# Optimization experiments

Measured on AMD Instinct MI355X. Metric: run time of the kernel, lower is better.

Reference implementation:

```python
import jax, jax.numpy as jnp
import numpy as np


def setup_inputs() -> dict:
    key = jax.random.key(0)
    ks = jax.random.split(key, 5)
    B, n_sites, d_bond, d_phys = 8192, 2048, 8, 2
    sr = n_sites // 2  # single_rank
    x = jax.random.normal(ks[0], (B, n_sites, d_phys), dtype=jnp.float32)
    scale = 0.01
    left_b = scale * jax.random.normal(ks[1], (d_bond, d_phys), dtype=jnp.float32)
    left = scale * jax.random.normal(ks[2], (sr - 1, d_bond, d_bond, d_phys), dtype=jnp.float32)
    right = scale * jax.random.normal(ks[3], (sr - 1, d_bond, d_bond, d_phys), dtype=jnp.float32)
    right_b = scale * jax.random.normal(ks[4], (d_bond, d_phys), dtype=jnp.float32)
    return {"x": x, "left_b": left_b, "left": left, "right": right, "right_b": right_b}


def reference(x, left_b, left, right, right_b):
    # x: [B, n_sites, d_phys]; left/right: [sr-1, bond, bond, d_phys]; boundaries: [bond, d_phys]
    n_sites = x.shape[1]
    sr = n_sites // 2

    # In-place slice normalizations performed at the top of call()
    left_b = left_b.at[2].set(left_b[2] / jnp.linalg.norm(left_b[2]))
    left = left.at[3].set(left[3] / jnp.linalg.norm(left[3]))
    right = right.at[3].set(right[3] / jnp.linalg.norm(right[3]))
    right_b = right_b.at[2].set(right_b[2] / jnp.linalg.norm(right_b[2]))

    # Left half: boundary phys contraction -> [B, bond]
    lvec = jnp.einsum("ap,kp->ka", left_b, x[:, 0])
    # Middle left: contract site-stack and phys axes -> [B, bond, bond]
    Lmat = jnp.einsum("sabp,ksp->kab", left, x[:, 1:sr])
    l = jnp.einsum("ka,kab->kb", lvec, Lmat)  # contract lb_n[0]^ln[1]

    # Right half (mirror)
    rvec = jnp.einsum("ap,kp->ka", right_b, x[:, n_sites - 1])
    Rmat = jnp.einsum("sabp,ksp->kab", right, x[:, sr : n_sites - 1])
    r = jnp.einsum("ka,kab->kb", rvec, Rmat)

    # Join halves: ln[2]^rn[2] -> scalar per sample, shape [B]
    return jnp.einsum("kb,kb->k", l, r)
```

## Files before the change

kernel.cpp:

```cpp
#include <hip/hip_runtime.h>
#include <hip/hip_bf16.h>

typedef __bf16  bf16x8  __attribute__((ext_vector_type(8)));
typedef float   floatx4 __attribute__((ext_vector_type(4)));

#define ROWLEN      4096
#define B_SAMPLES   8192
#define FRAG_ELEMS  (2*64*4*64*8)


__global__ __launch_bounds__(256) void repack_kernel(
    const float* __restrict__ left, const float* __restrict__ right,
    __bf16* __restrict__ wfrag)
{
    __shared__ float norms[2];
    const int tid  = threadIdx.x;
    const int wv   = tid >> 6;
    const int ln   = tid & 63;

    if (wv < 2) {
        const float* W = (wv == 0) ? left : right;
        float a = W[384 + ln], b = W[384 + 64 + ln];
        float s = a * a + b * b;
        s += __shfl_xor(s, 1);  s += __shfl_xor(s, 2);  s += __shfl_xor(s, 4);
        s += __shfl_xor(s, 8);  s += __shfl_xor(s, 16); s += __shfl_xor(s, 32);
        if (ln == 0) norms[wv] = 1.0f / sqrtf(s);
    }
    __syncthreads();
    const float invL = norms[0];
    const float invR = norms[1];

    const int g    = (int)(blockIdx.x * 256) + tid;
    const int lane = g & 63;
    const int nt   = (g >> 6) & 3;
    const int t    = (g >> 8) & 63;
    const int h    = (g >> 14) & 1;
    const int kk0  = t * 32 + (lane >> 4) * 8;
    const int n    = nt * 16 + (lane & 15);
    const int a    = n >> 3, bb = n & 7;
    const float* W = (h == 0) ? left : right;

    bf16x8 frag;
#pragma unroll
    for (int si = 0; si < 4; ++si) {
        const int kk = kk0 + si * 2;
        int s;  bool valid;
        if (h == 0) { s = (kk >> 1) - 1; valid = (kk >= 2); }
        else        { s = (kk >> 1);     valid = (s < 1023); }
        float w0 = 0.f, w1 = 0.f;
        if (valid) {
            const float* wp = W + ((s * 8 + a) * 8 + bb) * 2;
            w0 = wp[0]; w1 = wp[1];
            if (s == 3) { const float sc = (h == 0) ? invL : invR; w0 *= sc; w1 *= sc; }
        }
        frag[si * 2]     = (__bf16)w0;
        frag[si * 2 + 1] = (__bf16)w1;
    }
    ((bf16x8*)wfrag)[g] = frag;
}

__global__ __launch_bounds__(512, 4) void mps_main_kernel(
    const float* __restrict__ x, const __bf16* __restrict__ wfrag,
    const float* __restrict__ left_b, const float* __restrict__ right_b,
    float* __restrict__ out)
{
    __shared__ float lds[2][4][16][65];
    const int tid  = threadIdx.x;
    const int wid  = tid >> 6;
    const int lane = tid & 63;
    const int h    = wid & 1;
    const int c    = wid >> 1;
    const int mcol = lane & 15;
    const int q    = lane >> 4;
    const int blk  = blockIdx.x;

    const float* arow = x + (size_t)(blk * 16 + mcol) * ROWLEN
                          + h * 2048 + c * 512 + q * 8;
    const bf16x8* bbase = (const bf16x8*)wfrag
                          + ((size_t)(h * 64 + c * 16) * 4) * 64 + lane;

    floatx4 acc0 = {0.f,0.f,0.f,0.f}, acc1 = {0.f,0.f,0.f,0.f};
    floatx4 acc2 = {0.f,0.f,0.f,0.f}, acc3 = {0.f,0.f,0.f,0.f};

#pragma unroll 2
    for (int tl = 0; tl < 16; ++tl) {
        const floatx4* ap = (const floatx4*)(arow + tl * 32);
        const floatx4 a0 = __builtin_nontemporal_load(ap);
        const floatx4 a1 = __builtin_nontemporal_load(ap + 1);
        bf16x8 af;
        af[0] = (__bf16)a0[0]; af[1] = (__bf16)a0[1];
        af[2] = (__bf16)a0[2]; af[3] = (__bf16)a0[3];
        af[4] = (__bf16)a1[0]; af[5] = (__bf16)a1[1];
        af[6] = (__bf16)a1[2]; af[7] = (__bf16)a1[3];
        const bf16x8* bp = bbase + (size_t)tl * 256;
        const bf16x8 w0 = bp[0], w1 = bp[64], w2 = bp[128], w3 = bp[192];
        acc0 = __builtin_amdgcn_mfma_f32_16x16x32_bf16(af, w0, acc0, 0, 0, 0);
        acc1 = __builtin_amdgcn_mfma_f32_16x16x32_bf16(af, w1, acc1, 0, 0, 0);
        acc2 = __builtin_amdgcn_mfma_f32_16x16x32_bf16(af, w2, acc2, 0, 0, 0);
        acc3 = __builtin_amdgcn_mfma_f32_16x16x32_bf16(af, w3, acc3, 0, 0, 0);
    }

#pragma unroll
    for (int i = 0; i < 4; ++i) {
        const int r0 = q * 4 + i;
        lds[h][c][r0][ 0 + mcol] = acc0[i];
        lds[h][c][r0][16 + mcol] = acc1[i];
        lds[h][c][r0][32 + mcol] = acc2[i];
        lds[h][c][r0][48 + mcol] = acc3[i];
    }
    __syncthreads();

    if (tid < 128) {
        const int mm = tid >> 3;
        const int b  = tid & 7;
        const size_t k = (size_t)blk * 16 + mm;
        const float* xr = x + k * ROWLEN;
        const float x0 = xr[0],    x1 = xr[1];
        const float y0 = xr[4094], y1 = xr[4095];
        const float lbn = 1.0f / sqrtf(left_b[4]*left_b[4] + left_b[5]*left_b[5]);
        const float rbn = 1.0f / sqrtf(right_b[4]*right_b[4] + right_b[5]*right_b[5]);
        float l = 0.f, r = 0.f;
#pragma unroll
        for (int a = 0; a < 8; ++a) {
            float lv = left_b[a*2]  * x0 + left_b[a*2+1]  * x1;
            float rv = right_b[a*2] * y0 + right_b[a*2+1] * y1;
            if (a == 2) { lv *= lbn; rv *= rbn; }
            const int n = a * 8 + b;
            const float ls = lds[0][0][mm][n] + lds[0][1][mm][n]
                           + lds[0][2][mm][n] + lds[0][3][mm][n];
            const float rs = lds[1][0][mm][n] + lds[1][1][mm][n]
                           + lds[1][2][mm][n] + lds[1][3][mm][n];
            l += lv * ls;
            r += rv * rs;
        }
        float vv = l * r;
        vv += __shfl_xor(vv, 1);
        vv += __shfl_xor(vv, 2);
        vv += __shfl_xor(vv, 4);
        if (b == 0) out[k] = vv;
    }
}

extern "C" void kernel_launch(void* const* d_in, const int* in_sizes, int n_in,
                              void* d_out, int out_size, void* d_ws, size_t ws_size,
                              hipStream_t stream)
{
    const float* x       = (const float*)d_in[0];
    const float* left_b  = (const float*)d_in[1];
    const float* left    = (const float*)d_in[2];
    const float* right   = (const float*)d_in[3];
    const float* right_b = (const float*)d_in[4];

    __bf16* wfrag = (__bf16*)d_ws;
    float*  out   = (float*)d_out;

    hipLaunchKernelGGL(repack_kernel, dim3(128), dim3(256), 0, stream,
                       left, right, wfrag);
    hipLaunchKernelGGL(mps_main_kernel, dim3(B_SAMPLES / 16), dim3(512), 0, stream,
                       x, wfrag, left_b, right_b, out);
}
```

Measured before the change: 208.5 us.

## Stage x tiles into LDS with async global_load_lds double buffering

The main kernel now copies the x tile for each quarter-row into a double-buffered LDS buffer using direct global-to-LDS loads with XOR swizzling. The copy of the next chunk overlaps with MFMA compute on the current one. Work across waves changes from a split over halves and K to a split over N-tile and K-half, so the partial sums to reduce drop from four to two. LDS use grows to 128KB per block and launch bounds fall to 2 blocks per SM, which lowers occupancy and adds barrier synchronisation.

```diff
diff --git a/kernel.cpp b/kernel.cpp
--- a/kernel.cpp
+++ b/kernel.cpp
@@ -6,7 +6,13 @@
 
 #define ROWLEN      4096
 #define B_SAMPLES   8192
-#define FRAG_ELEMS  (2*64*4*64*8)
+
+typedef const __attribute__((address_space(1))) void* gas1_t;
+typedef __attribute__((address_space(3))) void*       las3_t;
+
+__device__ __forceinline__ void stage16(const float* g, float* l) {
+    __builtin_amdgcn_global_load_lds((gas1_t)g, (las3_t)l, 16, 0, 0);
+}
 
 
 __global__ __launch_bounds__(256) void repack_kernel(
@@ -59,61 +65,97 @@
     ((bf16x8*)wfrag)[g] = frag;
 }
 
-__global__ __launch_bounds__(512, 4) void mps_main_kernel(
+__global__ __launch_bounds__(512, 2) void mps_main_kernel(
     const float* __restrict__ x, const __bf16* __restrict__ wfrag,
     const float* __restrict__ left_b, const float* __restrict__ right_b,
     float* __restrict__ out)
 {
-    __shared__ float lds[2][4][16][65];
+    __shared__ float buf[2][16][1024];
     const int tid  = threadIdx.x;
     const int wid  = tid >> 6;
     const int lane = tid & 63;
-    const int h    = wid & 1;
-    const int c    = wid >> 1;
+    const int ntp  = wid & 3;
+    const int kkp  = wid >> 2;
     const int mcol = lane & 15;
     const int q    = lane >> 4;
+    const int sx   = mcol & 7;
     const int blk  = blockIdx.x;
 
-    const float* arow = x + (size_t)(blk * 16 + mcol) * ROWLEN
-                          + h * 2048 + c * 512 + q * 8;
-    const bf16x8* bbase = (const bf16x8*)wfrag
-                          + ((size_t)(h * 64 + c * 16) * 4) * 64 + lane;
-
-    floatx4 acc0 = {0.f,0.f,0.f,0.f}, acc1 = {0.f,0.f,0.f,0.f};
-    floatx4 acc2 = {0.f,0.f,0.f,0.f}, acc3 = {0.f,0.f,0.f,0.f};
-
-#pragma unroll 2
-    for (int tl = 0; tl < 16; ++tl) {
-        const floatx4* ap = (const floatx4*)(arow + tl * 32);
-        const floatx4 a0 = __builtin_nontemporal_load(ap);
-        const floatx4 a1 = __builtin_nontemporal_load(ap + 1);
-        bf16x8 af;
-        af[0] = (__bf16)a0[0]; af[1] = (__bf16)a0[1];
-        af[2] = (__bf16)a0[2]; af[3] = (__bf16)a0[3];
-        af[4] = (__bf16)a1[0]; af[5] = (__bf16)a1[1];
-        af[6] = (__bf16)a1[2]; af[7] = (__bf16)a1[3];
-        const bf16x8* bp = bbase + (size_t)tl * 256;
-        const bf16x8 w0 = bp[0], w1 = bp[64], w2 = bp[128], w3 = bp[192];
-        acc0 = __builtin_amdgcn_mfma_f32_16x16x32_bf16(af, w0, acc0, 0, 0, 0);
-        acc1 = __builtin_amdgcn_mfma_f32_16x16x32_bf16(af, w1, acc1, 0, 0, 0);
-        acc2 = __builtin_amdgcn_mfma_f32_16x16x32_bf16(af, w2, acc2, 0, 0, 0);
-        acc3 = __builtin_amdgcn_mfma_f32_16x16x32_bf16(af, w3, acc3, 0, 0, 0);
-    }
-
+    const float* xblk = x + (size_t)blk * 16 * ROWLEN;
+    const bf16x8* wf  = (const bf16x8*)wfrag;
+
+    auto STAGE = [&](int w, int b) {
+#pragma unroll
+        for (int rr = 0; rr < 2; ++rr) {
+            const int r = 2 * wid + rr;
+            const int sxor = r & 7;
+            const float* grow = xblk + (size_t)r * ROWLEN + w * 1024;
+#pragma unroll
+            for (int gi = 0; gi < 4; ++gi) {
+                const float* gp = grow + (gi * 64 + (lane ^ sxor)) * 4;
+                stage16(gp, &buf[b][r][gi * 256]);
+            }
+        }
+    };
+
+    floatx4 accL = {0.f,0.f,0.f,0.f};
+    floatx4 accR = {0.f,0.f,0.f,0.f};
+
+    auto COMPUTE = [&](int w, int b, floatx4& acc) {
+        const int h = w >> 1;
+#pragma unroll
+        for (int g4 = 0; g4 < 4; ++g4) {
+            bf16x8 wv[4];
+#pragma unroll
+            for (int j = 0; j < 4; ++j) {
+                const int t = (w & 1) * 32 + kkp * 16 + g4 * 4 + j;
+                wv[j] = wf[((size_t)((h * 64 + t) * 4 + ntp)) * 64 + lane];
+            }
+#pragma unroll
+            for (int j = 0; j < 4; ++j) {
+                const int tl = g4 * 4 + j;
+                const int gg = kkp * 128 + tl * 8 + 2 * q;
+                const floatx4 a0 = *(const floatx4*)&buf[b][mcol][((gg    ) ^ sx) * 4];
+                const floatx4 a1 = *(const floatx4*)&buf[b][mcol][((gg + 1) ^ sx) * 4];
+                bf16x8 af;
+                af[0] = (__bf16)a0[0]; af[1] = (__bf16)a0[1];
+                af[2] = (__bf16)a0[2]; af[3] = (__bf16)a0[3];
+                af[4] = (__bf16)a1[0]; af[5] = (__bf16)a1[1];
+                af[6] = (__bf16)a1[2]; af[7] = (__bf16)a1[3];
+                acc = __builtin_amdgcn_mfma_f32_16x16x32_bf16(af, wv[j], acc, 0, 0, 0);
+            }
+        }
+    };
+
+    STAGE(0, 0);
+
+#pragma unroll
+    for (int p = 0; p < 4; ++p) {
+        if (p < 3) STAGE(p + 1, (p + 1) & 1);
+        __builtin_amdgcn_sched_barrier(0);
+        if (p < 3) asm volatile("s_waitcnt vmcnt(8)" ::: "memory");
+        else       asm volatile("s_waitcnt vmcnt(0)" ::: "memory");
+        __builtin_amdgcn_s_barrier();
+        __builtin_amdgcn_sched_barrier(0);
+        if (p < 2) COMPUTE(p, p & 1, accL);
+        else       COMPUTE(p, p & 1, accR);
+        __builtin_amdgcn_sched_barrier(0);
+        __builtin_amdgcn_s_barrier();
+    }
+
+    float* red = &buf[0][0][0];
 #pragma unroll
     for (int i = 0; i < 4; ++i) {
-        const int r0 = q * 4 + i;
-        lds[h][c][r0][ 0 + mcol] = acc0[i];
-        lds[h][c][r0][16 + mcol] = acc1[i];
-        lds[h][c][r0][32 + mcol] = acc2[i];
-        lds[h][c][r0][48 + mcol] = acc3[i];
+        const int s = q * 4 + i;
+        red[((0 * 2 + kkp) * 16 + s) * 68 + ntp * 16 + mcol] = accL[i];
+        red[((1 * 2 + kkp) * 16 + s) * 68 + ntp * 16 + mcol] = accR[i];
     }
     __syncthreads();
 
     if (tid < 128) {
-        const int mm = tid >> 3;
-        const int b  = tid & 7;
-        const size_t k = (size_t)blk * 16 + mm;
+        const int s  = tid >> 3;
+        const int b2 = tid & 7;
+        const size_t k = (size_t)blk * 16 + s;
         const float* xr = x + k * ROWLEN;
         const float x0 = xr[0],    x1 = xr[1];
         const float y0 = xr[4094], y1 = xr[4095];
@@ -125,11 +167,9 @@
             float lv = left_b[a*2]  * x0 + left_b[a*2+1]  * x1;
             float rv = right_b[a*2] * y0 + right_b[a*2+1] * y1;
             if (a == 2) { lv *= lbn; rv *= rbn; }
-            const int n = a * 8 + b;
-            const float ls = lds[0][0][mm][n] + lds[0][1][mm][n]
-                           + lds[0][2][mm][n] + lds[0][3][mm][n];
-            const float rs = lds[1][0][mm][n] + lds[1][1][mm][n]
-                           + lds[1][2][mm][n] + lds[1][3][mm][n];
+            const int n = a * 8 + b2;
+            const float ls = red[((0*2+0)*16 + s)*68 + n] + red[((0*2+1)*16 + s)*68 + n];
+            const float rs = red[((1*2+0)*16 + s)*68 + n] + red[((1*2+1)*16 + s)*68 + n];
             l += lv * ls;
             r += rv * rs;
         }
@@ -137,7 +177,7 @@
         vv += __shfl_xor(vv, 1);
         vv += __shfl_xor(vv, 2);
         vv += __shfl_xor(vv, 4);
-        if (b == 0) out[k] = vv;
+        if (b2 == 0) out[k] = vv;
     }
 }
 
```

After: 209.6 us. No clear change (+0.5%).
